# Kernel tuning notes

Hardware: AMD Instinct MI355X
Metric: run time of the kernel (lower is better)

The kernel has to match this reference:

```python
import jax, jax.numpy as jnp
import numpy as np

NUM_HEADS = 8
HEAD_DIM = 64
HIDDEN = 512
ROPE_THETA = 500000.0


def _make_rope(seq_len, head_dim, theta):
    inv_freq = 1.0 / (theta ** (np.arange(0, head_dim, 2, dtype=np.float32) / head_dim))
    t = np.arange(seq_len, dtype=np.float32)
    freqs = np.outer(t, inv_freq)                  # [S, hd/2]
    emb = np.concatenate([freqs, freqs], axis=-1)  # [S, hd]
    return jnp.asarray(np.cos(emb)), jnp.asarray(np.sin(emb))


def setup_inputs() -> dict:
    key = jax.random.key(0)
    ks = jax.random.split(key, 5)
    B, S, H = 1, 4096, HIDDEN
    num_registers = 32
    hidden_states = jax.random.normal(ks[0], (B, S, H), dtype=jnp.float32)
    scale = 0.02
    Wq = jax.random.normal(ks[1], (H, H), dtype=jnp.float32) * scale
    Wk = jax.random.normal(ks[2], (H, H), dtype=jnp.float32) * scale
    Wv = jax.random.normal(ks[3], (H, H), dtype=jnp.float32) * scale
    Wo = jax.random.normal(ks[4], (H, H), dtype=jnp.float32) * scale
    cos, sin = _make_rope(S - num_registers, HEAD_DIM, ROPE_THETA)
    return {"hidden_states": hidden_states, "Wq": Wq, "Wk": Wk, "Wv": Wv,
            "Wo": Wo, "cos": cos, "sin": sin, "num_registers": num_registers}


def _rotate_half(x):
    x1, x2 = jnp.split(x, 2, axis=-1)
    return jnp.concatenate([-x2, x1], axis=-1)


def _apply_rope(q, k, cos, sin):
    # cos/sin: [S_real, hd] broadcast over [B, H, S_real, hd]
    cos = cos[None, None]
    sin = sin[None, None]
    return q * cos + _rotate_half(q) * sin, k * cos + _rotate_half(k) * sin


def reference(hidden_states, Wq, Wk, Wv, Wo, cos, sin, num_registers):
    B, S, _ = hidden_states.shape
    def proj(W):
        # torch Linear: x @ W.T -> [B, S, H] -> [B, nh, S, hd]
        y = jnp.einsum('bsh,oh->bso', hidden_states, W)
        return y.reshape(B, S, NUM_HEADS, HEAD_DIM).transpose(0, 2, 1, 3)
    q, k, v = proj(Wq), proj(Wk), proj(Wv)

    if num_registers > 0:
        q_reg, q_real = q[:, :, :num_registers], q[:, :, num_registers:]
        k_reg, k_real = k[:, :, :num_registers], k[:, :, num_registers:]
        q_real, k_real = _apply_rope(q_real, k_real, cos, sin)
        q = jnp.concatenate([q_reg, q_real], axis=2)
        k = jnp.concatenate([k_reg, k_real], axis=2)
    else:
        q, k = _apply_rope(q, k, cos, sin)

    scale = 1.0 / jnp.sqrt(jnp.float32(HEAD_DIM))
    scores = jnp.einsum('bhqd,bhkd->bhqk', q, k) * scale  # [B, nh, S, S]
    causal = jnp.tril(jnp.ones((S, S), dtype=bool))
    scores = jnp.where(causal[None, None], scores, jnp.float32(-1e30))
    attn = jax.nn.softmax(scores, axis=-1)
    out = jnp.einsum('bhqk,bhkd->bhqd', attn, v)
    out = out.transpose(0, 2, 1, 3).reshape(B, S, HIDDEN)
    return jnp.einsum('bsh,oh->bso', out, Wo)
```

## Files before the change

### kernel.cpp

```cpp
#include <hip/hip_runtime.h>
#include <cstdint>
#include <cstddef>

#define S_LEN 4096
#define HID   512
#define NHEAD 8
#define HD    64
#define SCALE_LOG2E 0.1803368801111204f

typedef __bf16 bf16;
typedef __bf16 bf16x8 __attribute__((ext_vector_type(8)));
typedef __bf16 bf16x4 __attribute__((ext_vector_type(4)));
typedef float  f32x4  __attribute__((ext_vector_type(4)));

__device__ __forceinline__ bf16x8 cvt8(float4 a, float4 b) {
    bf16x8 o;
    o[0] = (bf16)a.x; o[1] = (bf16)a.y; o[2] = (bf16)a.z; o[3] = (bf16)a.w;
    o[4] = (bf16)b.x; o[5] = (bf16)b.y; o[6] = (bf16)b.z; o[7] = (bf16)b.w;
    return o;
}

__global__ __launch_bounds__(256) void gemm_qkv(
    const float* __restrict__ Xf,
    const float* __restrict__ W0, const float* __restrict__ W1, const float* __restrict__ W2,
    const float* __restrict__ cosT, const float* __restrict__ sinT,
    const int* __restrict__ nregp,
    bf16* __restrict__ Qh, bf16* __restrict__ Kh, bf16* __restrict__ Vt)
{
    const int z = blockIdx.z;
    const float* W = (z == 0) ? W0 : (z == 1 ? W1 : W2);
    const int m0 = blockIdx.y * 64, n0 = blockIdx.x * 128;
    __shared__ bf16 lA[64][8][8];
    __shared__ bf16 lB[128][8][8];
    const int tid = threadIdx.x;
    const int lane = tid & 63, w = tid >> 6;
    const int l16 = lane & 15, lc = lane >> 4, l7 = lane & 7;
    const int wm = (w & 1) * 32, wn = (w >> 1) * 64;
    f32x4 acc[2][4] = {};

    for (int k0 = 0; k0 < HID; k0 += 64) {
        __syncthreads();
#pragma unroll
        for (int i = 0; i < 2; i++) {
            int uu = tid + 256 * i;
            int m = uu >> 3, c = uu & 7;
            const float* p = Xf + (size_t)(m0 + m) * HID + k0 + 8 * c;
            *(bf16x8*)(&lA[m][c ^ (m & 7)][0]) =
                cvt8(*(const float4*)p, *(const float4*)(p + 4));
        }
#pragma unroll
        for (int i = 0; i < 4; i++) {
            int uu = tid + 256 * i;
            int m = uu >> 3, c = uu & 7;
            const float* p = W + (size_t)(n0 + m) * HID + k0 + 8 * c;
            *(bf16x8*)(&lB[m][c ^ (m & 7)][0]) =
                cvt8(*(const float4*)p, *(const float4*)(p + 4));
        }
        __syncthreads();
#pragma unroll
        for (int ks = 0; ks < 2; ks++) {
            bf16x8 af[2], bfr[4];
#pragma unroll
            for (int i = 0; i < 2; i++)
                af[i]  = *(const bf16x8*)(&lA[wm + 16 * i + l16][(4 * ks + lc) ^ l7][0]);
#pragma unroll
            for (int j = 0; j < 4; j++)
                bfr[j] = *(const bf16x8*)(&lB[wn + 16 * j + l16][(4 * ks + lc) ^ l7][0]);
#pragma unroll
            for (int i = 0; i < 2; i++)
#pragma unroll
                for (int j = 0; j < 4; j++)
                    acc[i][j] = __builtin_amdgcn_mfma_f32_16x16x32_bf16(
                        af[i], bfr[j], acc[i][j], 0, 0, 0);
        }
    }

    const int h = (n0 + wn) >> 6;
    if (z == 2) {
#pragma unroll
        for (int i = 0; i < 2; i++) {
            const int s0r = m0 + wm + 16 * i + 4 * lc;
#pragma unroll
            for (int j = 0; j < 4; j++) {
                const int dl = 16 * j + l16;
                bf16x4 o;
#pragma unroll
                for (int r = 0; r < 4; r++) o[r] = (bf16)acc[i][j][r];
                *(bf16x4*)(Vt + ((size_t)(h * HD + dl)) * S_LEN + s0r) = o;
            }
        }
    } else {
        const int nreg = *nregp;
        bf16* dst = (z == 0) ? Qh : Kh;
#pragma unroll
        for (int i = 0; i < 2; i++) {
            const int s0r = m0 + wm + 16 * i + 4 * lc;
#pragma unroll
            for (int r = 0; r < 4; r++) {
                const int s = s0r + r;
                float c0 = 1.f, sn0 = 0.f, c1 = 1.f, sn1 = 0.f;
                if (s >= nreg) {
                    const int p = s - nreg;
                    c0  = cosT[(size_t)p * HD + l16];
                    sn0 = sinT[(size_t)p * HD + l16];
                    c1  = cosT[(size_t)p * HD + 16 + l16];
                    sn1 = sinT[(size_t)p * HD + 16 + l16];
                }
                const float x0 = acc[i][0][r], x1 = acc[i][1][r];
                const float x2 = acc[i][2][r], x3 = acc[i][3][r];
                bf16* row = dst + ((size_t)h * S_LEN + s) * HD;
                row[l16]      = (bf16)(x0 * c0 - x2 * sn0);
                row[l16 + 16] = (bf16)(x1 * c1 - x3 * sn1);
                row[l16 + 32] = (bf16)(x2 * c0 + x0 * sn0);
                row[l16 + 48] = (bf16)(x3 * c1 + x1 * sn1);
            }
        }
    }
}

__global__ __launch_bounds__(256) void gemm_out(
    const bf16* __restrict__ X, const float* __restrict__ Wf,
    float* __restrict__ Y)
{
    const int m0 = blockIdx.y * 64, n0 = blockIdx.x * 64;
    __shared__ bf16 lA[64][8][8];
    __shared__ bf16 lB[64][8][8];
    const int tid = threadIdx.x;
    const int lane = tid & 63, w = tid >> 6;
    const int l16 = lane & 15, lc = lane >> 4, l7 = lane & 7;
    const int wm = (w & 1) * 32, wn = (w >> 1) * 32;
    f32x4 acc[2][2] = {};

    for (int k0 = 0; k0 < HID; k0 += 64) {
        __syncthreads();
#pragma unroll
        for (int i = 0; i < 2; i++) {
            int uu = tid + 256 * i;
            int m = uu >> 3, c = uu & 7;
            *(bf16x8*)(&lA[m][c ^ (m & 7)][0]) =
                *(const bf16x8*)(X + (size_t)(m0 + m) * HID + k0 + 8 * c);
        }
#pragma unroll
        for (int i = 0; i < 2; i++) {
            int uu = tid + 256 * i;
            int m = uu >> 3, c = uu & 7;
            const float* p = Wf + (size_t)(n0 + m) * HID + k0 + 8 * c;
            *(bf16x8*)(&lB[m][c ^ (m & 7)][0]) =
                cvt8(*(const float4*)p, *(const float4*)(p + 4));
        }
        __syncthreads();
#pragma unroll
        for (int ks = 0; ks < 2; ks++) {
            bf16x8 af[2], bfr[2];
#pragma unroll
            for (int i = 0; i < 2; i++) {
                af[i]  = *(const bf16x8*)(&lA[wm + 16 * i + l16][(4 * ks + lc) ^ l7][0]);
                bfr[i] = *(const bf16x8*)(&lB[wn + 16 * i + l16][(4 * ks + lc) ^ l7][0]);
            }
#pragma unroll
            for (int i = 0; i < 2; i++)
#pragma unroll
                for (int j = 0; j < 2; j++)
                    acc[i][j] = __builtin_amdgcn_mfma_f32_16x16x32_bf16(
                        af[i], bfr[j], acc[i][j], 0, 0, 0);
        }
    }
#pragma unroll
    for (int i = 0; i < 2; i++) {
        int row = m0 + wm + 16 * i + 4 * lc;
#pragma unroll
        for (int j = 0; j < 2; j++) {
            int col = n0 + wn + 16 * j + l16;
#pragma unroll
            for (int r = 0; r < 4; r++)
                Y[(size_t)(row + r) * HID + col] = acc[i][j][r];
        }
    }
}

__global__ __launch_bounds__(256, 3) void attn_part(
    const bf16* __restrict__ Qh, const bf16* __restrict__ Kh,
    const bf16* __restrict__ Vt, float* __restrict__ Opart,
    float* __restrict__ Lpart)
{
    const int h = blockIdx.x >> 2;
    const int ch = blockIdx.x & 3;
    const int qb = 31 - (int)blockIdx.y;
    const int nkt = 2 * qb + 2;
    const int k0 = (nkt * ch) >> 2;
    const int k1 = (nkt * (ch + 1)) >> 2;
    const int tid = threadIdx.x;
    const int lane = tid & 63, w = tid >> 6;
    const int l16 = lane & 15, lc = lane >> 4, l7 = lane & 7;

    float* Op = Opart + ((size_t)((h * 32 + qb) * 4 + ch)) * 8192;
    float* Lp = Lpart + ((size_t)((h * 32 + qb) * 4 + ch)) * 128;

    if (k0 >= k1) {
        const f32x4 z = {0.f, 0.f, 0.f, 0.f};
#pragma unroll
        for (int i = 0; i < 8; i++)
            *(f32x4*)(Op + 4 * (tid + 256 * i)) = z;
        if (tid < 128) Lp[tid] = 0.f;
        return;
    }

    __shared__ bf16 lK[2][64][8][8];
    __shared__ bf16 lV[2][64][8][8];
    __shared__ bf16 lPT[4][2][16][76];

    const bf16* Kb_ = Kh + (size_t)h * S_LEN * HD;
    const bf16* Vb_ = Vt + (size_t)h * HD * S_LEN;

    int srow[2], scol[2];
#pragma unroll
    for (int i = 0; i < 2; i++) {
        int uu = tid + 256 * i;
        srow[i] = uu >> 3;
        scol[i] = uu & 7;
    }

    bf16x8 qf[2][2];
#pragma unroll
    for (int g = 0; g < 2; g++) {
        const bf16* qrow = Qh + (size_t)h * S_LEN * HD +
                           (size_t)(qb * 128 + g * 64 + 16 * w + l16) * HD;
        qf[g][0] = *(const bf16x8*)(qrow + 8 * lc);
        qf[g][1] = *(const bf16x8*)(qrow + 32 + 8 * lc);
    }
    f32x4 oacc[2][4] = {};
    float l_sum[2] = {0.f, 0.f};

    {
        bf16x8 kr[2], vr[2];
#pragma unroll
        for (int i = 0; i < 2; i++) {
            kr[i] = *(const bf16x8*)(Kb_ + (size_t)(k0 * 64 + srow[i]) * HD + 8 * scol[i]);
            vr[i] = *(const bf16x8*)(Vb_ + (size_t)srow[i] * S_LEN + k0 * 64 + 8 * scol[i]);
        }
#pragma unroll
        for (int i = 0; i < 2; i++) {
            *(bf16x8*)(&lK[0][srow[i]][scol[i] ^ (srow[i] & 7)][0]) = kr[i];
            *(bf16x8*)(&lV[0][srow[i]][scol[i] ^ (srow[i] & 7)][0]) = vr[i];
        }
    }

    int cur = 0;
    for (int kt = k0; kt < k1; kt++) {
        __syncthreads();

        bf16x8 kr[2], vr[2];
        if (kt + 1 < k1) {
#pragma unroll
            for (int i = 0; i < 2; i++) {
                kr[i] = *(const bf16x8*)(Kb_ + (size_t)((kt + 1) * 64 + srow[i]) * HD +
                                         8 * scol[i]);
                vr[i] = *(const bf16x8*)(Vb_ + (size_t)srow[i] * S_LEN +
                                         (kt + 1) * 64 + 8 * scol[i]);
            }
        }

        f32x4 s0[4] = {}, s1[4] = {};
#pragma unroll
        for (int ks = 0; ks < 2; ks++)
#pragma unroll
            for (int j = 0; j < 4; j++) {
                bf16x8 kf = *(const bf16x8*)(&lK[cur][16 * j + l16][(4 * ks + lc) ^ l7][0]);
                s0[j] = __builtin_amdgcn_mfma_f32_16x16x32_bf16(kf, qf[0][ks], s0[j], 0, 0, 0);
                s1[j] = __builtin_amdgcn_mfma_f32_16x16x32_bf16(kf, qf[1][ks], s1[j], 0, 0, 0);
            }

        const bool near_diag = (kt >= nkt - 2);
#pragma unroll
        for (int g = 0; g < 2; g++) {
            const f32x4* sg = g ? s1 : s0;
            float pv[4][4];
#pragma unroll
            for (int j = 0; j < 4; j++)
#pragma unroll
                for (int r = 0; r < 4; r++)
                    pv[j][r] = __builtin_amdgcn_exp2f(sg[j][r] * SCALE_LOG2E);
            if (near_diag) {
                const int qg = qb * 128 + g * 64 + 16 * w + l16;
#pragma unroll
                for (int j = 0; j < 4; j++)
#pragma unroll
                    for (int r = 0; r < 4; r++) {
                        const int keyg = kt * 64 + 16 * j + 4 * lc + r;
                        if (keyg > qg) pv[j][r] = 0.f;
                    }
            }
#pragma unroll
            for (int j = 0; j < 4; j++)
                l_sum[g] += (pv[j][0] + pv[j][1]) + (pv[j][2] + pv[j][3]);
#pragma unroll
            for (int j = 0; j < 4; j++) {
                bf16x4 pp;
#pragma unroll
                for (int r = 0; r < 4; r++) pp[r] = (bf16)pv[j][r];
                *(bf16x4*)(&lPT[w][g][l16][16 * j + 4 * lc]) = pp;
            }
        }

        bf16x8 pb[2][2];
#pragma unroll
        for (int g = 0; g < 2; g++)
#pragma unroll
            for (int ks = 0; ks < 2; ks++)
                pb[g][ks] = *(const bf16x8*)(&lPT[w][g][l16][32 * ks + 8 * lc]);
#pragma unroll
        for (int ks = 0; ks < 2; ks++)
#pragma unroll
            for (int j = 0; j < 4; j++) {
                bf16x8 vf = *(const bf16x8*)(&lV[cur][16 * j + l16][(4 * ks + lc) ^ l7][0]);
                oacc[0][j] = __builtin_amdgcn_mfma_f32_16x16x32_bf16(
                    vf, pb[0][ks], oacc[0][j], 0, 0, 0);
                oacc[1][j] = __builtin_amdgcn_mfma_f32_16x16x32_bf16(
                    vf, pb[1][ks], oacc[1][j], 0, 0, 0);
            }

        if (kt + 1 < k1) {
#pragma unroll
            for (int i = 0; i < 2; i++) {
                *(bf16x8*)(&lK[cur ^ 1][srow[i]][scol[i] ^ (srow[i] & 7)][0]) = kr[i];
                *(bf16x8*)(&lV[cur ^ 1][srow[i]][scol[i] ^ (srow[i] & 7)][0]) = vr[i];
            }
        }
        cur ^= 1;
    }

#pragma unroll
    for (int g = 0; g < 2; g++) {
        float ls = l_sum[g];
        ls += __shfl_xor(ls, 16, 64);
        ls += __shfl_xor(ls, 32, 64);
        if (lane < 16) Lp[g * 64 + 16 * w + l16] = ls;
#pragma unroll
        for (int j = 0; j < 4; j++)
            *(f32x4*)(Op + (size_t)(g * 64 + 16 * w + l16) * 64 + 16 * j + 4 * lc) =
                oacc[g][j];
    }
}

__global__ __launch_bounds__(256) void attn_combine(
    const float* __restrict__ Opart, const float* __restrict__ Lpart,
    bf16* __restrict__ Ob)
{
    const int h = blockIdx.x, qb = blockIdx.y;
    const size_t base = (size_t)((h * 32 + qb) * 4);
    const float* O0 = Opart + base * 8192;
    const float* L0 = Lpart + base * 128;
    const int t = threadIdx.x;
    const int q = t >> 1, dh = (t & 1) * 32;
    const float l = (L0[q] + L0[128 + q]) + (L0[256 + q] + L0[384 + q]);
    const float inv = 1.0f / l;
    bf16* out = Ob + (size_t)(qb * 128 + q) * HID + h * HD + dh;
#pragma unroll
    for (int g = 0; g < 4; g++) {
        const int off = q * 64 + dh + 8 * g;
        bf16x8 o8;
#pragma unroll
        for (int e = 0; e < 2; e++) {
            f32x4 a = *(const f32x4*)(O0 + off + 4 * e);
            f32x4 b = *(const f32x4*)(O0 + 8192 + off + 4 * e);
            f32x4 c = *(const f32x4*)(O0 + 16384 + off + 4 * e);
            f32x4 d = *(const f32x4*)(O0 + 24576 + off + 4 * e);
#pragma unroll
            for (int r = 0; r < 4; r++)
                o8[4 * e + r] = (bf16)(((a[r] + b[r]) + (c[r] + d[r])) * inv);
        }
        *(bf16x8*)(out + 8 * g) = o8;
    }
}

extern "C" void kernel_launch(void* const* d_in, const int* in_sizes, int n_in,
                              void* d_out, int out_size, void* d_ws, size_t ws_size,
                              hipStream_t stream) {
    const float* hs   = (const float*)d_in[0];
    const float* Wq   = (const float*)d_in[1];
    const float* Wk   = (const float*)d_in[2];
    const float* Wv   = (const float*)d_in[3];
    const float* Wo   = (const float*)d_in[4];
    const float* cosT = (const float*)d_in[5];
    const float* sinT = (const float*)d_in[6];
    const int*   nreg = (const int*)d_in[7];

    char* ws = (char*)d_ws;
    const size_t MiB = 1 << 20;
    bf16*  Qh    = (bf16*)(ws);
    bf16*  Kh    = (bf16*)(ws + 4 * MiB);
    bf16*  Vt    = (bf16*)(ws + 8 * MiB);
    bf16*  Ob    = (bf16*)(ws + 12 * MiB);
    float* Opart = (float*)(ws + 16 * MiB);
    float* Lpart = (float*)(ws + 50 * MiB);

    gemm_qkv<<<dim3(4, 64, 3), 256, 0, stream>>>(hs, Wq, Wk, Wv,
                                                 cosT, sinT, nreg, Qh, Kh, Vt);
    attn_part<<<dim3(32, 32), 256, 0, stream>>>(Qh, Kh, Vt, Opart, Lpart);
    attn_combine<<<dim3(8, 32), 256, 0, stream>>>(Opart, Lpart, Ob);
    gemm_out<<<dim3(8, 64), 256, 0, stream>>>(Ob, Wo, (float*)d_out);
}
```

Before: 152.3 us.

## Pre-convert inputs to bf16, stage Q/K stores through LDS, fuse combine into out-proj

Adds a cvt_in kernel that converts the hidden states and all four weight matrices to bf16 once, so the GEMMs load bf16 directly. gemm_qkv now stages the RoPE'd Q/K tile in shared memory and writes coalesced 16-byte rows. Attention split-K drops from 4 chunks to 2, and the partial-combine kernel is fused into the output projection, which normalises partials while loading its A tile. This removes one launch and the Ob round trip but adds a conversion pass and halves attention parallelism.

```diff
diff --git a/kernel.cpp b/kernel.cpp
--- a/kernel.cpp
+++ b/kernel.cpp
@@ -13,25 +13,42 @@
 typedef __bf16 bf16x4 __attribute__((ext_vector_type(4)));
 typedef float  f32x4  __attribute__((ext_vector_type(4)));
 
-__device__ __forceinline__ bf16x8 cvt8(float4 a, float4 b) {
-    bf16x8 o;
-    o[0] = (bf16)a.x; o[1] = (bf16)a.y; o[2] = (bf16)a.z; o[3] = (bf16)a.w;
-    o[4] = (bf16)b.x; o[5] = (bf16)b.y; o[6] = (bf16)b.z; o[7] = (bf16)b.w;
-    return o;
+__global__ __launch_bounds__(256) void cvt_in(
+    const float* __restrict__ hs, const float* __restrict__ wq,
+    const float* __restrict__ wk, const float* __restrict__ wv,
+    const float* __restrict__ wo,
+    bf16* __restrict__ xb, bf16* __restrict__ wqb, bf16* __restrict__ wkb,
+    bf16* __restrict__ wvb, bf16* __restrict__ wob)
+{
+    int e = (blockIdx.x * 256 + threadIdx.x) * 4;
+    const float* s; bf16* d; int o;
+    if (e < 2 * 1024 * 1024) { s = hs; d = xb; o = e; }
+    else {
+        int t = e - 2 * 1024 * 1024;
+        int wi = t >> 18;
+        o = t & ((1 << 18) - 1);
+        s = (wi == 0) ? wq : (wi == 1) ? wk : (wi == 2) ? wv : wo;
+        d = (wi == 0) ? wqb : (wi == 1) ? wkb : (wi == 2) ? wvb : wob;
+    }
+    const float4 v = *(const float4*)(s + o);
+    bf16x4 ob;
+    ob[0] = (bf16)v.x; ob[1] = (bf16)v.y; ob[2] = (bf16)v.z; ob[3] = (bf16)v.w;
+    *(bf16x4*)(d + o) = ob;
 }
 
 __global__ __launch_bounds__(256) void gemm_qkv(
-    const float* __restrict__ Xf,
-    const float* __restrict__ W0, const float* __restrict__ W1, const float* __restrict__ W2,
+    const bf16* __restrict__ Xb,
+    const bf16* __restrict__ W0, const bf16* __restrict__ W1, const bf16* __restrict__ W2,
     const float* __restrict__ cosT, const float* __restrict__ sinT,
     const int* __restrict__ nregp,
     bf16* __restrict__ Qh, bf16* __restrict__ Kh, bf16* __restrict__ Vt)
 {
     const int z = blockIdx.z;
-    const float* W = (z == 0) ? W0 : (z == 1 ? W1 : W2);
+    const bf16* W = (z == 0) ? W0 : (z == 1 ? W1 : W2);
     const int m0 = blockIdx.y * 64, n0 = blockIdx.x * 128;
     __shared__ bf16 lA[64][8][8];
     __shared__ bf16 lB[128][8][8];
+    __shared__ bf16 scratch[64][136];
     const int tid = threadIdx.x;
     const int lane = tid & 63, w = tid >> 6;
     const int l16 = lane & 15, lc = lane >> 4, l7 = lane & 7;
@@ -44,17 +61,15 @@
         for (int i = 0; i < 2; i++) {
             int uu = tid + 256 * i;
             int m = uu >> 3, c = uu & 7;
-            const float* p = Xf + (size_t)(m0 + m) * HID + k0 + 8 * c;
             *(bf16x8*)(&lA[m][c ^ (m & 7)][0]) =
-                cvt8(*(const float4*)p, *(const float4*)(p + 4));
+                *(const bf16x8*)(Xb + (size_t)(m0 + m) * HID + k0 + 8 * c);
         }
 #pragma unroll
         for (int i = 0; i < 4; i++) {
             int uu = tid + 256 * i;
             int m = uu >> 3, c = uu & 7;
-            const float* p = W + (size_t)(n0 + m) * HID + k0 + 8 * c;
             *(bf16x8*)(&lB[m][c ^ (m & 7)][0]) =
-                cvt8(*(const float4*)p, *(const float4*)(p + 4));
+                *(const bf16x8*)(W + (size_t)(n0 + m) * HID + k0 + 8 * c);
         }
         __syncthreads();
 #pragma unroll
@@ -75,8 +90,8 @@
         }
     }
 
-    const int h = (n0 + wn) >> 6;
     if (z == 2) {
+        const int h = (n0 + wn) >> 6;
 #pragma unroll
         for (int i = 0; i < 2; i++) {
             const int s0r = m0 + wm + 16 * i + 4 * lc;
@@ -94,10 +109,10 @@
         bf16* dst = (z == 0) ? Qh : Kh;
 #pragma unroll
         for (int i = 0; i < 2; i++) {
-            const int s0r = m0 + wm + 16 * i + 4 * lc;
+            const int sl0 = wm + 16 * i + 4 * lc;
 #pragma unroll
             for (int r = 0; r < 4; r++) {
-                const int s = s0r + r;
+                const int s = m0 + sl0 + r;
                 float c0 = 1.f, sn0 = 0.f, c1 = 1.f, sn1 = 0.f;
                 if (s >= nreg) {
                     const int p = s - nreg;
@@ -108,102 +123,44 @@
                 }
                 const float x0 = acc[i][0][r], x1 = acc[i][1][r];
                 const float x2 = acc[i][2][r], x3 = acc[i][3][r];
-                bf16* row = dst + ((size_t)h * S_LEN + s) * HD;
+                bf16* row = &scratch[sl0 + r][wn];
                 row[l16]      = (bf16)(x0 * c0 - x2 * sn0);
                 row[l16 + 16] = (bf16)(x1 * c1 - x3 * sn1);
                 row[l16 + 32] = (bf16)(x2 * c0 + x0 * sn0);
                 row[l16 + 48] = (bf16)(x3 * c1 + x1 * sn1);
             }
         }
+        __syncthreads();
+        const int h0 = n0 >> 6;
+#pragma unroll
+        for (int i = 0; i < 4; i++) {
+            int u = tid + 256 * i;
+            int row = u >> 4, c = u & 15;
+            bf16x8 val = *(const bf16x8*)(&scratch[row][c * 8]);
+            *(bf16x8*)(dst + ((size_t)(h0 + (c >> 3)) * S_LEN + m0 + row) * HD +
+                       (c & 7) * 8) = val;
+        }
     }
 }
 
-__global__ __launch_bounds__(256) void gemm_out(
-    const bf16* __restrict__ X, const float* __restrict__ Wf,
-    float* __restrict__ Y)
-{
-    const int m0 = blockIdx.y * 64, n0 = blockIdx.x * 64;
-    __shared__ bf16 lA[64][8][8];
-    __shared__ bf16 lB[64][8][8];
-    const int tid = threadIdx.x;
-    const int lane = tid & 63, w = tid >> 6;
-    const int l16 = lane & 15, lc = lane >> 4, l7 = lane & 7;
-    const int wm = (w & 1) * 32, wn = (w >> 1) * 32;
-    f32x4 acc[2][2] = {};
-
-    for (int k0 = 0; k0 < HID; k0 += 64) {
-        __syncthreads();
-#pragma unroll
-        for (int i = 0; i < 2; i++) {
-            int uu = tid + 256 * i;
-            int m = uu >> 3, c = uu & 7;
-            *(bf16x8*)(&lA[m][c ^ (m & 7)][0]) =
-                *(const bf16x8*)(X + (size_t)(m0 + m) * HID + k0 + 8 * c);
-        }
-#pragma unroll
-        for (int i = 0; i < 2; i++) {
-            int uu = tid + 256 * i;
-            int m = uu >> 3, c = uu & 7;
-            const float* p = Wf + (size_t)(n0 + m) * HID + k0 + 8 * c;
-            *(bf16x8*)(&lB[m][c ^ (m & 7)][0]) =
-                cvt8(*(const float4*)p, *(const float4*)(p + 4));
-        }
-        __syncthreads();
-#pragma unroll
-        for (int ks = 0; ks < 2; ks++) {
-            bf16x8 af[2], bfr[2];
-#pragma unroll
-            for (int i = 0; i < 2; i++) {
-                af[i]  = *(const bf16x8*)(&lA[wm + 16 * i + l16][(4 * ks + lc) ^ l7][0]);
-                bfr[i] = *(const bf16x8*)(&lB[wn + 16 * i + l16][(4 * ks + lc) ^ l7][0]);
-            }
-#pragma unroll
-            for (int i = 0; i < 2; i++)
-#pragma unroll
-                for (int j = 0; j < 2; j++)
-                    acc[i][j] = __builtin_amdgcn_mfma_f32_16x16x32_bf16(
-                        af[i], bfr[j], acc[i][j], 0, 0, 0);
-        }
-    }
-#pragma unroll
-    for (int i = 0; i < 2; i++) {
-        int row = m0 + wm + 16 * i + 4 * lc;
-#pragma unroll
-        for (int j = 0; j < 2; j++) {
-            int col = n0 + wn + 16 * j + l16;
-#pragma unroll
-            for (int r = 0; r < 4; r++)
-                Y[(size_t)(row + r) * HID + col] = acc[i][j][r];
-        }
-    }
-}
-
-__global__ __launch_bounds__(256, 3) void attn_part(
+__global__ __launch_bounds__(256, 2) void attn_part(
     const bf16* __restrict__ Qh, const bf16* __restrict__ Kh,
     const bf16* __restrict__ Vt, float* __restrict__ Opart,
     float* __restrict__ Lpart)
 {
-    const int h = blockIdx.x >> 2;
-    const int ch = blockIdx.x & 3;
+    const int h = blockIdx.x >> 1;
+    const int ch = blockIdx.x & 1;
     const int qb = 31 - (int)blockIdx.y;
     const int nkt = 2 * qb + 2;
-    const int k0 = (nkt * ch) >> 2;
-    const int k1 = (nkt * (ch + 1)) >> 2;
+    const int kmid = nkt >> 1;
+    const int k0 = ch ? kmid : 0;
+    const int k1 = ch ? nkt : kmid;
     const int tid = threadIdx.x;
     const int lane = tid & 63, w = tid >> 6;
     const int l16 = lane & 15, lc = lane >> 4, l7 = lane & 7;
 
-    float* Op = Opart + ((size_t)((h * 32 + qb) * 4 + ch)) * 8192;
-    float* Lp = Lpart + ((size_t)((h * 32 + qb) * 4 + ch)) * 128;
-
-    if (k0 >= k1) {
-        const f32x4 z = {0.f, 0.f, 0.f, 0.f};
-#pragma unroll
-        for (int i = 0; i < 8; i++)
-            *(f32x4*)(Op + 4 * (tid + 256 * i)) = z;
-        if (tid < 128) Lp[tid] = 0.f;
-        return;
-    }
+    float* Op = Opart + ((size_t)((h * 32 + qb) * 2 + ch)) * 8192;
+    float* Lp = Lpart + ((size_t)((h * 32 + qb) * 2 + ch)) * 128;
 
     __shared__ bf16 lK[2][64][8][8];
     __shared__ bf16 lV[2][64][8][8];
@@ -342,34 +299,78 @@
     }
 }
 
-__global__ __launch_bounds__(256) void attn_combine(
+__global__ __launch_bounds__(256) void gemm_out_f(
     const float* __restrict__ Opart, const float* __restrict__ Lpart,
-    bf16* __restrict__ Ob)
+    const bf16* __restrict__ Wb, float* __restrict__ Y)
 {
-    const int h = blockIdx.x, qb = blockIdx.y;
-    const size_t base = (size_t)((h * 32 + qb) * 4);
-    const float* O0 = Opart + base * 8192;
-    const float* L0 = Lpart + base * 128;
-    const int t = threadIdx.x;
-    const int q = t >> 1, dh = (t & 1) * 32;
-    const float l = (L0[q] + L0[128 + q]) + (L0[256 + q] + L0[384 + q]);
-    const float inv = 1.0f / l;
-    bf16* out = Ob + (size_t)(qb * 128 + q) * HID + h * HD + dh;
-#pragma unroll
-    for (int g = 0; g < 4; g++) {
-        const int off = q * 64 + dh + 8 * g;
-        bf16x8 o8;
-#pragma unroll
-        for (int e = 0; e < 2; e++) {
-            f32x4 a = *(const f32x4*)(O0 + off + 4 * e);
-            f32x4 b = *(const f32x4*)(O0 + 8192 + off + 4 * e);
-            f32x4 c = *(const f32x4*)(O0 + 16384 + off + 4 * e);
-            f32x4 d = *(const f32x4*)(O0 + 24576 + off + 4 * e);
+    const int by = blockIdx.y;
+    const int m0 = by * 64, n0 = blockIdx.x * 64;
+    const int qb = by >> 1, qloc0 = (by & 1) * 64;
+    __shared__ bf16 lA[64][8][8];
+    __shared__ bf16 lB[64][8][8];
+    __shared__ float Linv[8][64];
+    const int tid = threadIdx.x;
+    const int lane = tid & 63, w = tid >> 6;
+    const int l16 = lane & 15, lc = lane >> 4, l7 = lane & 7;
+    const int wm = (w & 1) * 32, wn = (w >> 1) * 32;
+
+    for (int e = tid; e < 512; e += 256) {
+        const int hh = e >> 6, m = e & 63;
+        const float* Lp = Lpart + ((size_t)(hh * 32 + qb) * 2) * 128 + qloc0 + m;
+        Linv[hh][m] = 1.0f / (Lp[0] + Lp[128]);
+    }
+
+    f32x4 acc[2][2] = {};
+    for (int k0 = 0; k0 < HID; k0 += 64) {
+        const int hh = k0 >> 6;
+        const float* Ph = Opart + ((size_t)(hh * 32 + qb) * 2) * 8192;
+        __syncthreads();
+#pragma unroll
+        for (int i = 0; i < 2; i++) {
+            int uu = tid + 256 * i;
+            int m = uu >> 3, c = uu & 7;
+            const float* P0 = Ph + (size_t)(qloc0 + m) * 64 + 8 * c;
+            const float inv = Linv[hh][m];
+            bf16x8 o;
+#pragma unroll
+            for (int e2 = 0; e2 < 8; e2++)
+                o[e2] = (bf16)((P0[e2] + P0[8192 + e2]) * inv);
+            *(bf16x8*)(&lA[m][c ^ (m & 7)][0]) = o;
+        }
+#pragma unroll
+        for (int i = 0; i < 2; i++) {
+            int uu = tid + 256 * i;
+            int m = uu >> 3, c = uu & 7;
+            *(bf16x8*)(&lB[m][c ^ (m & 7)][0]) =
+                *(const bf16x8*)(Wb + (size_t)(n0 + m) * HID + k0 + 8 * c);
+        }
+        __syncthreads();
+#pragma unroll
+        for (int ks = 0; ks < 2; ks++) {
+            bf16x8 af[2], bfr[2];
+#pragma unroll
+            for (int i = 0; i < 2; i++) {
+                af[i]  = *(const bf16x8*)(&lA[wm + 16 * i + l16][(4 * ks + lc) ^ l7][0]);
+                bfr[i] = *(const bf16x8*)(&lB[wn + 16 * i + l16][(4 * ks + lc) ^ l7][0]);
+            }
+#pragma unroll
+            for (int i = 0; i < 2; i++)
+#pragma unroll
+                for (int j = 0; j < 2; j++)
+                    acc[i][j] = __builtin_amdgcn_mfma_f32_16x16x32_bf16(
+                        af[i], bfr[j], acc[i][j], 0, 0, 0);
+        }
+    }
+#pragma unroll
+    for (int i = 0; i < 2; i++) {
+        int row = m0 + wm + 16 * i + 4 * lc;
+#pragma unroll
+        for (int j = 0; j < 2; j++) {
+            int col = n0 + wn + 16 * j + l16;
 #pragma unroll
             for (int r = 0; r < 4; r++)
-                o8[4 * e + r] = (bf16)(((a[r] + b[r]) + (c[r] + d[r])) * inv);
-        }
-        *(bf16x8*)(out + 8 * g) = o8;
+                Y[(size_t)(row + r) * HID + col] = acc[i][j][r];
+        }
     }
 }
 
@@ -390,13 +391,17 @@
     bf16*  Qh    = (bf16*)(ws);
     bf16*  Kh    = (bf16*)(ws + 4 * MiB);
     bf16*  Vt    = (bf16*)(ws + 8 * MiB);
-    bf16*  Ob    = (bf16*)(ws + 12 * MiB);
     float* Opart = (float*)(ws + 16 * MiB);
-    float* Lpart = (float*)(ws + 50 * MiB);
-
-    gemm_qkv<<<dim3(4, 64, 3), 256, 0, stream>>>(hs, Wq, Wk, Wv,
+    float* Lpart = (float*)(ws + 32 * MiB);
+    bf16*  Xb    = (bf16*)(ws + 33 * MiB);
+    bf16*  Wqb   = (bf16*)(ws + 37 * MiB);
+    bf16*  Wkb   = (bf16*)(ws + 37 * MiB + 512 * 1024);
+    bf16*  Wvb   = (bf16*)(ws + 38 * MiB);
+    bf16*  Wob   = (bf16*)(ws + 38 * MiB + 512 * 1024);
+
+    cvt_in<<<3072, 256, 0, stream>>>(hs, Wq, Wk, Wv, Wo, Xb, Wqb, Wkb, Wvb, Wob);
+    gemm_qkv<<<dim3(4, 64, 3), 256, 0, stream>>>(Xb, Wqb, Wkb, Wvb,
                                                  cosT, sinT, nreg, Qh, Kh, Vt);
-    attn_part<<<dim3(32, 32), 256, 0, stream>>>(Qh, Kh, Vt, Opart, Lpart);
-    attn_combine<<<dim3(8, 32), 256, 0, stream>>>(Opart, Lpart, Ob);
-    gemm_out<<<dim3(8, 64), 256, 0, stream>>>(Ob, Wo, (float*)d_out);
+    attn_part<<<dim3(16, 32), 256, 0, stream>>>(Qh, Kh, Vt, Opart, Lpart);
+    gemm_out_f<<<dim3(8, 64), 256, 0, stream>>>(Opart, Lpart, Wob, (float*)d_out);
 }
```

Result: slower. 156.8 us (+3.0%).
